# Kernel optimization log

Hardware: AMD Instinct MI355X
Metric: run time of the kernel (lower is better)

Reference implementation:

```python
import jax, jax.numpy as jnp
import numpy as np

B, NQ, L, E, K = 64, 1024, 128, 8192, 2
LN_EPS = 1e-5


def setup_inputs() -> dict:
    key = jax.random.key(0)
    ks = jax.random.split(key, 16)
    s1 = 1.0 / np.sqrt(2 * L + 1)
    s2 = 1.0 / np.sqrt(L)
    s3 = 1.0 / np.sqrt(2 * L)
    return {
        "z0": jax.random.normal(ks[0], (B, L), jnp.float32),
        "edge_index": jax.random.randint(ks[1], (2, E), 0, NQ, jnp.int64),
        "edge_attr": jax.random.normal(ks[2], (E,), jnp.float32),
        "n_qubits": NQ,
        # edge MLP params, stacked over K message-passing rounds
        "e_w1": jax.random.normal(ks[3], (K, L, 2 * L + 1), jnp.float32) * s1,
        "e_b1": jnp.zeros((K, L), jnp.float32),
        "e_w2": jax.random.normal(ks[4], (K, L, L), jnp.float32) * s2,
        "e_b2": jnp.zeros((K, L), jnp.float32),
        # node MLP params
        "n_w1": jax.random.normal(ks[5], (K, L, 2 * L), jnp.float32) * s3,
        "n_b1": jnp.zeros((K, L), jnp.float32),
        "ln_g": jnp.ones((K, L), jnp.float32),
        "ln_b": jnp.zeros((K, L), jnp.float32),
        "n_w2": jax.random.normal(ks[6], (K, L, L), jnp.float32) * s2,
        "n_b2": jnp.zeros((K, L), jnp.float32),
    }


def reference(z0, edge_index, edge_attr, n_qubits,
              e_w1, e_b1, e_w2, e_b2,
              n_w1, n_b1, ln_g, ln_b, n_w2, n_b2):
    b, l = z0.shape
    src, tgt = edge_index[0], edge_index[1]
    e_ = src.shape[0]
    # broadcast latent z0 to every node: h [B, N, L]
    h = jnp.broadcast_to(z0[:, None, :], (b, n_qubits, l))
    e = jnp.broadcast_to(edge_attr[None, :, None], (b, e_, 1))  # [B, E, 1]
    k_rounds = e_w1.shape[0]
    for k in range(k_rounds):
        hi = h[:, src, :]  # gather source node feats [B, E, L]
        hj = h[:, tgt, :]  # gather target node feats [B, E, L]
        inp_e = jnp.concatenate([hi, hj, e], axis=-1)  # [B, E, 2L+1]
        m = jax.nn.relu(inp_e @ e_w1[k].T + e_b1[k]) @ e_w2[k].T + e_b2[k]
        # scatter_add messages back to source nodes
        m_agg = jnp.zeros_like(h).at[:, src, :].add(m)
        inp_n = jnp.concatenate([h, m_agg], axis=-1)  # [B, N, 2L]
        x = jax.nn.relu(inp_n @ n_w1[k].T + n_b1[k])
        mu = x.mean(axis=-1, keepdims=True)
        var = ((x - mu) ** 2).mean(axis=-1, keepdims=True)
        x = (x - mu) * jax.lax.rsqrt(var + LN_EPS) * ln_g[k] + ln_b[k]
        # Dropout(p=0.1) is identity in eval mode
        h = x @ n_w2[k].T + n_b2[k] + h  # residual
    return h.mean(axis=1)  # [B, L]
```

## Files before the change

kernel.cpp:

```cpp
#include <hip/hip_runtime.h>

#define B_   64
#define NQ_  1024
#define L_   128
#define E_   8192
#define M_   (B_*NQ_)
#define LDP  136
#define TILE 2176

typedef unsigned short u16;
typedef unsigned int   u32;
typedef __attribute__((ext_vector_type(8))) short short8;
typedef __attribute__((ext_vector_type(4))) float floatx4;

#define WVB() __builtin_amdgcn_wave_barrier()

__device__ __forceinline__ u16 f2bf(float f) {
    union { float f; u32 u; } v; v.f = f;
    return (u16)((v.u + 0x7fffu + ((v.u >> 16) & 1u)) >> 16);
}
__device__ __forceinline__ float bf2f(u16 u) {
    union { u32 u; float f; } v; v.u = ((u32)u) << 16;
    return v.f;
}
__device__ __forceinline__ floatx4 mfma16(short8 a, short8 b, floatx4 c) {
    return __builtin_amdgcn_mfma_f32_16x16x32_bf16(a, b, c, 0, 0, 0);
}
__device__ __forceinline__ short8 gfrag(const u16* base, int r0, int kb, int lane) {
    return *(const short8*)(base + (size_t)(r0 + (lane & 15)) * 128 + kb * 32 + (lane >> 4) * 8);
}
__device__ __forceinline__ short8 sfrag(const u16* t, int r0, int kb, int lane) {
    return *(const short8*)(t + (r0 + (lane & 15)) * LDP + kb * 32 + (lane >> 4) * 8);
}
__device__ __forceinline__ short8 wfrag(const u16* wf, int nt, int kb, int lane) {
    return *(const short8*)(wf + (((kb << 3) + nt) * 64 + lane) * 8);
}
__device__ __forceinline__ void frag_flush(const u16* t, u16* wf, int nt, int lane) {
#pragma unroll
    for (int kb = 0; kb < 4; ++kb)
        *(short8*)(wf + (((kb << 3) + nt) * 64 + lane) * 8) = sfrag(t, 0, kb, lane);
}
__device__ __forceinline__ short8 frag_cvt(const float* base, int r0, int ld, int kb, int lane) {
    const float* p = base + (size_t)(r0 + (lane & 15)) * ld + kb * 32 + (lane >> 4) * 8;
    short8 s;
#pragma unroll
    for (int j = 0; j < 8; ++j) s[j] = (short)f2bf(p[j]);
    return s;
}
__device__ __forceinline__ void tile_store(u16* t, const floatx4* acc, int lane) {
    int col = lane & 15, qd = lane >> 4;
#pragma unroll
    for (int nt = 0; nt < 8; ++nt)
#pragma unroll
        for (int r = 0; r < 4; ++r)
            t[(qd * 4 + r) * LDP + nt * 16 + col] = f2bf(acc[nt][r]);
}
__device__ __forceinline__ void tile_flush(const u16* t, u16* g, int lane) {
#pragma unroll
    for (int it = 0; it < 4; ++it) {
        int chunk = it * 64 + lane, row = chunk >> 4, c8 = chunk & 15;
        *(uint4*)(g + (size_t)row * 128 + c8 * 8) = *(const uint4*)(t + row * LDP + c8 * 8);
    }
}

struct P {
    const int* ei; const float* attr; const float* z0;
    const float* e_w1; const float* e_b1; const float* e_w2; const float* e_b2;
    const float* n_w1; const float* n_b1; const float* ln_g; const float* ln_b;
    const float* n_w2; const float* n_b2;
    int* ofs; int* tgt_s; float* a_s; float* degf;
    u16* wf;
    u16* w_n20;
    float* wl; float* vb2;
    float* rx; float* rci; float* rcj; float* rh; float* mx0;
    u16* c0t; u16* S; u16* t1g; u16* ci1; u16* cj1;
    float* out;
};

__global__ __launch_bounds__(256) void k_setup(P p) {
    __shared__ __align__(16) char smem[52224];
    int tid = threadIdx.x, blk = blockIdx.x;
    int lane = tid & 63, w = tid >> 6, col = lane & 15, qd = lane >> 4;

    if (blk == 0) {
        int* cnt  = (int*)smem;
        int* wsum = cnt + 1024;
        int* flag = wsum + 8;
#pragma unroll
        for (int i = 0; i < 4; ++i) cnt[tid + i * 256] = 0;
        if (tid == 0) *flag = 1;
        __syncthreads();
        if (tid < 100 && p.ei[2 * tid + 1] != 0) atomicAnd(flag, 0);
        __syncthreads();
        int i64 = *flag;
        for (int e = tid; e < E_; e += 256) {
            int s = i64 ? p.ei[2 * e] : p.ei[e];
            atomicAdd(&cnt[s], 1);
        }
        __syncthreads();
        int q0 = tid * 4;
        int c0 = cnt[q0], c1 = cnt[q0 + 1], c2 = cnt[q0 + 2], c3 = cnt[q0 + 3];
        int tsum = c0 + c1 + c2 + c3, incl = tsum;
#pragma unroll
        for (int o = 1; o < 64; o <<= 1) {
            int t = __shfl_up(incl, o, 64);
            if (lane >= o) incl += t;
        }
        if (lane == 63) wsum[w] = incl;
        __syncthreads();
        int wo = 0;
        for (int i = 0; i < w; ++i) wo += wsum[i];
        int base = wo + incl - tsum;
        p.ofs[q0] = base; p.ofs[q0 + 1] = base + c0;
        p.ofs[q0 + 2] = base + c0 + c1; p.ofs[q0 + 3] = base + c0 + c1 + c2;
        p.degf[q0] = (float)c0; p.degf[q0 + 1] = (float)c1;
        p.degf[q0 + 2] = (float)c2; p.degf[q0 + 3] = (float)c3;
        if (tid == 0) p.ofs[NQ_] = E_;
        __syncthreads();
        cnt[q0] = base; cnt[q0 + 1] = base + c0;
        cnt[q0 + 2] = base + c0 + c1; cnt[q0 + 3] = base + c0 + c1 + c2;
        __syncthreads();
        for (int e = tid; e < E_; e += 256) {
            int s = i64 ? p.ei[2 * e]        : p.ei[e];
            int t = i64 ? p.ei[2 * (E_ + e)] : p.ei[E_ + e];
            int pos = atomicAdd(&cnt[s], 1);
            p.tgt_s[pos] = t;
            p.a_s[pos]   = p.attr[e];
        }
    } else if (blk == 1) {
        for (int idx = tid; idx < 16384; idx += 256) p.w_n20[idx] = f2bf(p.n_w2[idx]);
    } else if (blk == 2) {
        const float* src = p.n_w2 + 16384;
        u16* dst = p.wf + 5 * 16384;
        for (int pr = w; pr < 32; pr += 4) {
            int kb = pr >> 3, nt = pr & 7;
            const float* s = src + (nt * 16 + (lane & 15)) * 128 + kb * 32 + (lane >> 4) * 8;
            short8 v;
#pragma unroll
            for (int j = 0; j < 8; ++j) v[j] = (short)f2bf(s[j]);
            *(short8*)(dst + (pr * 64 + lane) * 8) = v;
        }
    } else if (blk <= 7) {
        const float* Pm; const float* Q; int ldp; u16* D;
        switch (blk) {
            case 3: Pm = p.n_w1 + 128;             ldp = 256; Q = p.e_w2;         D = p.wf;             break;
            case 4: Pm = p.n_w1 + 32768 + 128;     ldp = 256; Q = p.e_w2 + 16384; D = p.wf + 4 * 16384; break;
            case 5: Pm = p.e_w1 + 128 * 257;       ldp = 257; Q = p.n_w2;         D = p.wf + 1 * 16384; break;
            case 6: Pm = p.e_w1 + 128 * 257 + 128; ldp = 257; Q = p.n_w2;         D = p.wf + 2 * 16384; break;
            default:Pm = p.n_w1 + 32768;           ldp = 256; Q = p.n_w2;         D = p.wf + 3 * 16384; break;
        }
        u16* qt = (u16*)smem;
        u16* tl = (u16*)(smem + 34816);
        for (int idx = tid; idx < 16384; idx += 256) {
            int c = idx >> 7, kd = idx & 127;
            qt[kd * LDP + c] = f2bf(Q[idx]);
        }
        __syncthreads();
        for (int t = 0; t < 2; ++t) {
            int r0 = (w * 2 + t) * 16;
            floatx4 acc[8] = {};
#pragma unroll
            for (int kb = 0; kb < 4; ++kb) {
                short8 a = frag_cvt(Pm, r0, ldp, kb, lane);
#pragma unroll
                for (int nt = 0; nt < 8; ++nt)
                    acc[nt] = mfma16(a, sfrag(qt, nt * 16, kb, lane), acc[nt]);
            }
            u16* slot = tl + w * TILE;
            tile_store(slot, acc, lane); WVB();
            frag_flush(slot, D, w * 2 + t, lane); WVB();
        }
    } else if (blk == 8) {
        int r0 = w * 16;
        floatx4 acc[8] = {};
#pragma unroll
        for (int kb = 0; kb < 4; ++kb) {
            short8 a = frag_cvt(p.z0, r0, 128, kb, lane);
#pragma unroll
            for (int nt = 0; nt < 8; ++nt)
                acc[nt] = mfma16(a, frag_cvt(p.n_w1, nt * 16, 256, kb, lane), acc[nt]);
        }
#pragma unroll
        for (int nt = 0; nt < 8; ++nt) {
            int cg = nt * 16 + col; float bv = p.n_b1[cg];
#pragma unroll
            for (int r = 0; r < 4; ++r) p.rx[(r0 + qd * 4 + r) * 128 + cg] = acc[nt][r] + bv;
        }
    } else if (blk <= 11) {
        int r0 = w * 16;
        const float* Wp; int ld; const float* bias; float* dst;
        if (blk == 9)       { Wp = p.e_w1 + 128 * 257;       ld = 257; bias = p.e_b1 + 128; dst = p.rci; }
        else if (blk == 10) { Wp = p.e_w1 + 128 * 257 + 128; ld = 257; bias = nullptr;      dst = p.rcj; }
        else                { Wp = p.n_w1 + 32768;           ld = 256; bias = p.n_b1 + 128; dst = p.rh;  }
        floatx4 acc[8] = {};
#pragma unroll
        for (int kb = 0; kb < 4; ++kb) {
            short8 a;
            int rr = (r0 + (lane & 15)) * 128, kk = kb * 32 + (lane >> 4) * 8;
#pragma unroll
            for (int j = 0; j < 8; ++j) a[j] = (short)f2bf(p.z0[rr + kk + j] + p.n_b2[kk + j]);
#pragma unroll
            for (int nt = 0; nt < 8; ++nt)
                acc[nt] = mfma16(a, frag_cvt(Wp, nt * 16, ld, kb, lane), acc[nt]);
        }
#pragma unroll
        for (int nt = 0; nt < 8; ++nt) {
            int cg = nt * 16 + col;
            float bv = bias ? bias[cg] : 0.0f;
#pragma unroll
            for (int r = 0; r < 4; ++r) dst[(r0 + qd * 4 + r) * 128 + cg] = acc[nt][r] + bv;
        }
    } else if (blk == 12) {
        u16* tl = (u16*)(smem + 34816);
        int r0 = w * 16;
        floatx4 a1[8] = {};
#pragma unroll
        for (int kb = 0; kb < 4; ++kb) {
            short8 a = frag_cvt(p.z0, r0, 128, kb, lane);
#pragma unroll
            for (int nt = 0; nt < 8; ++nt) {
                a1[nt] = mfma16(a, frag_cvt(p.e_w1,       nt * 16, 257, kb, lane), a1[nt]);
                a1[nt] = mfma16(a, frag_cvt(p.e_w1 + 128, nt * 16, 257, kb, lane), a1[nt]);
            }
        }
#pragma unroll
        for (int nt = 0; nt < 8; ++nt) {
            float bv = p.e_b1[nt * 16 + col];
#pragma unroll
            for (int r = 0; r < 4; ++r) a1[nt][r] += bv;
        }
        u16* slot = tl + w * TILE;
        tile_store(slot, a1, lane); WVB();
        tile_flush(slot, p.c0t + (size_t)r0 * 128, lane);
    } else if (blk == 13) {
        int k = tid >> 7, c = tid & 127;
        float s = 0.0f;
        for (int n = 0; n < 128; ++n)
            s += p.n_w1[k * 32768 + c * 256 + 128 + n] * p.e_b2[k * 128 + n];
        p.vb2[tid] = s;
        p.wl[tid]  = p.e_w1[k * 128 * 257 + c * 257 + 256];
        for (int i = tid; i < 8192; i += 256) p.mx0[i] = 0.0f;
    }
}

__global__ __launch_bounds__(256) void k_edge(P p) {
    int tid = threadIdx.x, lane = tid & 63, w = tid >> 6;
    const float* wl = p.wl + 128;
    float2 wl2 = ((const float2*)wl)[lane];
    int gw = blockIdx.x * 4 + w;
    int q = gw & (NQ_ - 1), bg = gw >> 10;
    int bl[8];
#pragma unroll
    for (int i = 0; i < 4; ++i) { bl[i] = bg * 4 + i; bl[i + 4] = bg * 4 + i + 32; }
    int st = p.ofs[q], en = p.ofs[q + 1];
    float ax[8] = {}, ay[8] = {};
    const u32* cjp[8];
    float cx[8], cy[8];
#pragma unroll
    for (int i = 0; i < 8; ++i) {
        cjp[i] = (const u32*)p.cj1 + (size_t)bl[i] * NQ_ * 64;
        u32 cv = ((const u32*)p.ci1)[((size_t)bl[i] * NQ_ + q) * 64 + lane];
        cx[i] = bf2f((u16)(cv & 0xffff)); cy[i] = bf2f((u16)(cv >> 16));
    }
    for (int idx = st; idx < en; ++idx) {
        int t = p.tgt_s[idx];
        float a = p.a_s[idx];
        size_t ro = (size_t)t * 64 + lane;
        float wx = a * wl2.x, wy = a * wl2.y;
#pragma unroll
        for (int i = 0; i < 8; ++i) {
            u32 jv = cjp[i][ro];
            ax[i] += fmaxf(cx[i] + bf2f((u16)(jv & 0xffff)) + wx, 0.f);
            ay[i] += fmaxf(cy[i] + bf2f((u16)(jv >> 16))    + wy, 0.f);
        }
    }
    u32* Sp = (u32*)p.S;
#pragma unroll
    for (int i = 0; i < 8; ++i)
        Sp[((size_t)bl[i] * NQ_ + q) * 64 + lane] =
            (u32)f2bf(ax[i]) | ((u32)f2bf(ay[i]) << 16);
}

__global__ __launch_bounds__(256, 2) void k_node0(P p) {
    __shared__ __align__(16) char smem[52224];
    u16* xt = (u16*)smem;
    u16* ob = (u16*)(smem + 34816);
    int tid = threadIdx.x, lane = tid & 63, w = tid >> 6;
    int col = lane & 15, qd = lane >> 4;
    int blk = blockIdx.x;
    int rowbase = blk * 128 + w * 32;
    int b = blk >> 3;

    short8 af[2][4];
    {
        float wlf[4][8], c0f[4][8];
#pragma unroll
        for (int kb = 0; kb < 4; ++kb) {
            const float* wp = p.wl + kb * 32 + qd * 8;
            const u16*  cp = p.c0t + b * 128 + kb * 32 + qd * 8;
#pragma unroll
            for (int j = 0; j < 8; ++j) { wlf[kb][j] = wp[j]; c0f[kb][j] = bf2f(cp[j]); }
        }
#pragma unroll
        for (int t = 0; t < 2; ++t) {
            int q = (rowbase + t * 16 + col) & (NQ_ - 1);
            int st = p.ofs[q], en = p.ofs[q + 1];
            float Sv[4][8] = {};
            for (int idx = st; idx < en; ++idx) {
                float a = p.a_s[idx];
#pragma unroll
                for (int kb = 0; kb < 4; ++kb)
#pragma unroll
                    for (int j = 0; j < 8; ++j)
                        Sv[kb][j] += fmaxf(fmaf(a, wlf[kb][j], c0f[kb][j]), 0.f);
            }
#pragma unroll
            for (int kb = 0; kb < 4; ++kb) {
                short8 v;
#pragma unroll
                for (int j = 0; j < 8; ++j) v[j] = (short)f2bf(Sv[kb][j]);
                af[t][kb] = v;
            }
        }
    }

    floatx4 xa[2][8] = {};
#pragma unroll
    for (int kb = 0; kb < 4; ++kb) {
        short8 Bv[8];
#pragma unroll
        for (int nt = 0; nt < 8; ++nt) Bv[nt] = wfrag(p.wf, nt, kb, lane);
#pragma unroll
        for (int t = 0; t < 2; ++t)
#pragma unroll
            for (int nt = 0; nt < 8; ++nt) xa[t][nt] = mfma16(af[t][kb], Bv[nt], xa[t][nt]);
    }
    float s8[8] = {};
#pragma unroll
    for (int t = 0; t < 2; ++t) {
#pragma unroll
        for (int nt = 0; nt < 8; ++nt) {
            int cg = nt * 16 + col;
            float base = p.rx[b * 128 + cg], vb = p.vb2[cg];
#pragma unroll
            for (int r = 0; r < 4; ++r) {
                int row = rowbase + t * 16 + qd * 4 + r;
                xa[t][nt][r] = fmaxf(xa[t][nt][r] + base + p.degf[row & (NQ_ - 1)] * vb, 0.f);
            }
        }
#pragma unroll
        for (int r = 0; r < 4; ++r) {
            float s = 0.f, s2 = 0.f;
#pragma unroll
            for (int nt = 0; nt < 8; ++nt) { float v = xa[t][nt][r]; s += v; s2 += v * v; }
#pragma unroll
            for (int o = 1; o < 16; o <<= 1) { s += __shfl_xor(s, o, 64); s2 += __shfl_xor(s2, o, 64); }
            float mu = s * (1.f / 128.f), var = s2 * (1.f / 128.f) - mu * mu;
            float rs = rsqrtf(var + 1e-5f);
#pragma unroll
            for (int nt = 0; nt < 8; ++nt) {
                int cg = nt * 16 + col;
                float xv = (xa[t][nt][r] - mu) * rs * p.ln_g[cg] + p.ln_b[cg];
                xa[t][nt][r] = xv;
                s8[nt] += xv;
            }
        }
        tile_store(xt + (w * 2 + t) * TILE, xa[t], lane);
    }
#pragma unroll
    for (int nt = 0; nt < 8; ++nt) {
        s8[nt] += __shfl_xor(s8[nt], 16, 64);
        s8[nt] += __shfl_xor(s8[nt], 32, 64);
    }
    if (lane < 16) {
#pragma unroll
        for (int nt = 0; nt < 8; ++nt)
            atomicAdd(p.mx0 + b * 128 + nt * 16 + lane, s8[nt]);
    }
    WVB();
#pragma unroll
    for (int ph = 0; ph < 3; ++ph) {
        const u16* wfp = p.wf + ((ph == 0) ? 1 : (ph == 1) ? 2 : 3) * 16384;
        const float* rt = (ph == 0) ? p.rci : (ph == 1) ? p.rcj : p.rh;
        floatx4 ca[2][8] = {};
#pragma unroll
        for (int kb = 0; kb < 4; ++kb) {
            short8 Bv[8];
#pragma unroll
            for (int nt = 0; nt < 8; ++nt) Bv[nt] = wfrag(wfp, nt, kb, lane);
#pragma unroll
            for (int t = 0; t < 2; ++t) {
                short8 a = sfrag(xt + (w * 2 + t) * TILE, 0, kb, lane);
#pragma unroll
                for (int nt = 0; nt < 8; ++nt) ca[t][nt] = mfma16(a, Bv[nt], ca[t][nt]);
            }
        }
#pragma unroll
        for (int t = 0; t < 2; ++t)
#pragma unroll
            for (int nt = 0; nt < 8; ++nt) {
                float rc = rt[b * 128 + nt * 16 + col];
#pragma unroll
                for (int r = 0; r < 4; ++r) ca[t][nt][r] += rc;
            }
        u16* dst = (ph == 0) ? p.ci1 : (ph == 1) ? p.cj1 : p.t1g;
#pragma unroll
        for (int t = 0; t < 2; ++t) {
            tile_store(ob + w * TILE, ca[t], lane);
            WVB();
            tile_flush(ob + w * TILE, dst + (size_t)(rowbase + t * 16) * 128, lane);
            WVB();
        }
    }
}

__global__ __launch_bounds__(256, 2) void k_node1(P p) {
    __shared__ __align__(16) char smem[52224];
    u16* ob = (u16*)(smem + 34816);
    int tid = threadIdx.x, lane = tid & 63, w = tid >> 6;
    int col = lane & 15, qd = lane >> 4;
    int blk = blockIdx.x;
    int rowbase = blk * 128 + w * 32;
    int b = blk >> 3;

    const u16* wc1 = p.wf + 4 * 16384;
    floatx4 xa[2][8] = {};
#pragma unroll
    for (int kb = 0; kb < 4; ++kb) {
        short8 Bv[8];
#pragma unroll
        for (int nt = 0; nt < 8; ++nt) Bv[nt] = wfrag(wc1, nt, kb, lane);
#pragma unroll
        for (int t = 0; t < 2; ++t) {
            short8 a = gfrag(p.S, rowbase + t * 16, kb, lane);
#pragma unroll
            for (int nt = 0; nt < 8; ++nt) xa[t][nt] = mfma16(a, Bv[nt], xa[t][nt]);
        }
    }
    const float* vb21 = p.vb2 + 128;
#pragma unroll
    for (int t = 0; t < 2; ++t) {
#pragma unroll
        for (int nt = 0; nt < 8; ++nt) {
            int cg = nt * 16 + col;
            float vb = vb21[cg];
#pragma unroll
            for (int r = 0; r < 4; ++r) {
                int row = rowbase + t * 16 + qd * 4 + r;
                float tv = bf2f(p.t1g[(size_t)row * 128 + cg]);
                xa[t][nt][r] = fmaxf(xa[t][nt][r] + tv + p.degf[row & (NQ_ - 1)] * vb, 0.f);
            }
        }
#pragma unroll
        for (int r = 0; r < 4; ++r) {
            float s = 0.f, s2 = 0.f;
#pragma unroll
            for (int nt = 0; nt < 8; ++nt) { float v = xa[t][nt][r]; s += v; s2 += v * v; }
#pragma unroll
            for (int o = 1; o < 16; o <<= 1) { s += __shfl_xor(s, o, 64); s2 += __shfl_xor(s2, o, 64); }
            float mu = s * (1.f / 128.f), var = s2 * (1.f / 128.f) - mu * mu;
            float rs = rsqrtf(var + 1e-5f);
#pragma unroll
            for (int nt = 0; nt < 8; ++nt) {
                int cg = nt * 16 + col;
                xa[t][nt][r] = (xa[t][nt][r] - mu) * rs * p.ln_g[128 + cg] + p.ln_b[128 + cg];
            }
        }
    }
    const u16* n21 = p.wf + 5 * 16384;
    float s8[8] = {};
#pragma unroll
    for (int t = 0; t < 2; ++t) {
        WVB();
        tile_store(ob + w * TILE, xa[t], lane);
        WVB();
        floatx4 ma[8] = {};
#pragma unroll
        for (int kb = 0; kb < 4; ++kb) {
            short8 Bv[8];
#pragma unroll
            for (int nt = 0; nt < 8; ++nt) Bv[nt] = wfrag(n21, nt, kb, lane);
            short8 a = sfrag(ob + w * TILE, 0, kb, lane);
#pragma unroll
            for (int nt = 0; nt < 8; ++nt) ma[nt] = mfma16(a, Bv[nt], ma[nt]);
        }
#pragma unroll
        for (int nt = 0; nt < 8; ++nt)
#pragma unroll
            for (int r = 0; r < 4; ++r) s8[nt] += ma[nt][r];
    }
#pragma unroll
    for (int nt = 0; nt < 8; ++nt) {
        s8[nt] += __shfl_xor(s8[nt], 16, 64);
        s8[nt] += __shfl_xor(s8[nt], 32, 64);
    }
    if (lane < 16) {
#pragma unroll
        for (int nt = 0; nt < 8; ++nt)
            atomicAdd(p.out + b * 128 + nt * 16 + lane, s8[nt] * (1.f / 1024.f));
    }
    if ((blk & 7) == 0 && tid < 128) {
        int c = tid;
        const float* mx = p.mx0 + b * 128;
        float s = 0.f;
#pragma unroll 4
        for (int k = 0; k < 128; ++k) s += mx[k] * bf2f(p.w_n20[c * 128 + k]);
        float acc = p.z0[b * 128 + c] + p.n_b2[c] + p.n_b2[128 + c] + s * (1.f / 1024.f);
        atomicAdd(p.out + b * 128 + c, acc);
    }
}

extern "C" void kernel_launch(void* const* d_in, const int* in_sizes, int n_in,
                              void* d_out, int out_size, void* d_ws, size_t ws_size,
                              hipStream_t stream) {
    P p;
    p.z0   = (const float*)d_in[0];
    p.ei   = (const int*)d_in[1];
    p.attr = (const float*)d_in[2];
    p.e_w1 = (const float*)d_in[4];
    p.e_b1 = (const float*)d_in[5];
    p.e_w2 = (const float*)d_in[6];
    p.e_b2 = (const float*)d_in[7];
    p.n_w1 = (const float*)d_in[8];
    p.n_b1 = (const float*)d_in[9];
    p.ln_g = (const float*)d_in[10];
    p.ln_b = (const float*)d_in[11];
    p.n_w2 = (const float*)d_in[12];
    p.n_b2 = (const float*)d_in[13];
    p.out  = (float*)d_out;

    const size_t H = (size_t)M_ * L_;
    float* f  = (float*)d_ws;
    p.degf = f;
    p.a_s  = f + 1024;
    p.wl   = p.a_s + 8192;
    p.vb2  = p.wl + 256;
    p.rx   = p.vb2 + 256;
    p.rci  = p.rx + 8192;
    p.rcj  = p.rci + 8192;
    p.rh   = p.rcj + 8192;
    p.mx0  = p.rh + 8192;
    p.ofs  = (int*)(p.mx0 + 8192);
    p.tgt_s = p.ofs + 1056;
    p.wf    = (u16*)(p.tgt_s + 8192);
    p.w_n20 = p.wf + 6 * 16384;
    p.c0t   = p.w_n20 + 16384;
    p.S     = p.c0t + 8192;
    p.t1g   = p.S + H;
    p.ci1   = p.t1g + H;
    p.cj1   = p.ci1 + H;

    hipMemsetAsync(p.out, 0, 8192 * sizeof(float), stream);

    k_setup<<<14, 256, 0, stream>>>(p);
    k_node0<<<512, 256, 0, stream>>>(p);
    k_edge<<<2048, 256, 0, stream>>>(p);
    k_node1<<<512, 256, 0, stream>>>(p);
}
```

Baseline: 191.7 us.

## Split setup work across more blocks and restructure node0 edge aggregation via LDS

The setup kernel grows from 14 to 20 blocks. The weight-product GEMMs are each split across two blocks, and the Q operand is now read directly from global memory rather than staged through shared memory. The bias-vector dot product is vectorized with float4, and the final mx·W reduction reads packed bf16 vectors. In node0, each lane now accumulates two feature columns per row across edges and writes the result to an LDS tile. The MFMA A operand is then read from that tile, replacing the per-lane 32-element register accumulation. The aim is to shorten the serial setup critical path and cut register pressure in node0, at the cost of more serial loop iterations per lane and extra LDS traffic.

```diff
diff --git a/kernel.cpp b/kernel.cpp
--- a/kernel.cpp
+++ b/kernel.cpp
@@ -78,21 +78,21 @@
 };
 
 __global__ __launch_bounds__(256) void k_setup(P p) {
-    __shared__ __align__(16) char smem[52224];
+    __shared__ __align__(16) char smem[17408];
     int tid = threadIdx.x, blk = blockIdx.x;
     int lane = tid & 63, w = tid >> 6, col = lane & 15, qd = lane >> 4;
 
     if (blk == 0) {
-        int* cnt  = (int*)smem;
-        int* wsum = cnt + 1024;
-        int* flag = wsum + 8;
+        __shared__ int cnt[1024];
+        __shared__ int wsum[4];
+        __shared__ int flag;
 #pragma unroll
         for (int i = 0; i < 4; ++i) cnt[tid + i * 256] = 0;
-        if (tid == 0) *flag = 1;
+        if (tid == 0) flag = 1;
         __syncthreads();
-        if (tid < 100 && p.ei[2 * tid + 1] != 0) atomicAnd(flag, 0);
+        if (tid < 100 && p.ei[2 * tid + 1] != 0) atomicAnd(&flag, 0);
         __syncthreads();
-        int i64 = *flag;
+        int i64 = flag;
         for (int e = tid; e < E_; e += 256) {
             int s = i64 ? p.ei[2 * e] : p.ei[e];
             atomicAdd(&cnt[s], 1);
@@ -127,50 +127,50 @@
             p.tgt_s[pos] = t;
             p.a_s[pos]   = p.attr[e];
         }
-    } else if (blk == 1) {
-        for (int idx = tid; idx < 16384; idx += 256) p.w_n20[idx] = f2bf(p.n_w2[idx]);
-    } else if (blk == 2) {
+    } else if (blk <= 2) {
+        int base = (blk - 1) * 8192;
+        for (int idx = tid; idx < 8192; idx += 256)
+            p.w_n20[base + idx] = f2bf(p.n_w2[base + idx]);
+    } else if (blk == 3) {
         const float* src = p.n_w2 + 16384;
         u16* dst = p.wf + 5 * 16384;
         for (int pr = w; pr < 32; pr += 4) {
             int kb = pr >> 3, nt = pr & 7;
-            const float* s = src + (nt * 16 + (lane & 15)) * 128 + kb * 32 + (lane >> 4) * 8;
+            const float* s = src + (nt * 16 + col) * 128 + kb * 32 + qd * 8;
             short8 v;
 #pragma unroll
             for (int j = 0; j < 8; ++j) v[j] = (short)f2bf(s[j]);
             *(short8*)(dst + (pr * 64 + lane) * 8) = v;
         }
-    } else if (blk <= 7) {
+    } else if (blk <= 13) {
+        int g = (blk - 4) >> 1, part = (blk - 4) & 1;
         const float* Pm; const float* Q; int ldp; u16* D;
-        switch (blk) {
-            case 3: Pm = p.n_w1 + 128;             ldp = 256; Q = p.e_w2;         D = p.wf;             break;
-            case 4: Pm = p.n_w1 + 32768 + 128;     ldp = 256; Q = p.e_w2 + 16384; D = p.wf + 4 * 16384; break;
-            case 5: Pm = p.e_w1 + 128 * 257;       ldp = 257; Q = p.n_w2;         D = p.wf + 1 * 16384; break;
-            case 6: Pm = p.e_w1 + 128 * 257 + 128; ldp = 257; Q = p.n_w2;         D = p.wf + 2 * 16384; break;
-            default:Pm = p.n_w1 + 32768;           ldp = 256; Q = p.n_w2;         D = p.wf + 3 * 16384; break;
-        }
-        u16* qt = (u16*)smem;
-        u16* tl = (u16*)(smem + 34816);
-        for (int idx = tid; idx < 16384; idx += 256) {
-            int c = idx >> 7, kd = idx & 127;
-            qt[kd * LDP + c] = f2bf(Q[idx]);
-        }
-        __syncthreads();
-        for (int t = 0; t < 2; ++t) {
-            int r0 = (w * 2 + t) * 16;
-            floatx4 acc[8] = {};
-#pragma unroll
-            for (int kb = 0; kb < 4; ++kb) {
-                short8 a = frag_cvt(Pm, r0, ldp, kb, lane);
-#pragma unroll
-                for (int nt = 0; nt < 8; ++nt)
-                    acc[nt] = mfma16(a, sfrag(qt, nt * 16, kb, lane), acc[nt]);
-            }
-            u16* slot = tl + w * TILE;
-            tile_store(slot, acc, lane); WVB();
-            frag_flush(slot, D, w * 2 + t, lane); WVB();
-        }
-    } else if (blk == 8) {
+        switch (g) {
+            case 0:  Pm = p.n_w1 + 128;             ldp = 256; Q = p.e_w2;         D = p.wf;             break;
+            case 1:  Pm = p.n_w1 + 32768 + 128;     ldp = 256; Q = p.e_w2 + 16384; D = p.wf + 4 * 16384; break;
+            case 2:  Pm = p.e_w1 + 128 * 257;       ldp = 257; Q = p.n_w2;         D = p.wf + 1 * 16384; break;
+            case 3:  Pm = p.e_w1 + 128 * 257 + 128; ldp = 257; Q = p.n_w2;         D = p.wf + 2 * 16384; break;
+            default: Pm = p.n_w1 + 32768;           ldp = 256; Q = p.n_w2;         D = p.wf + 3 * 16384; break;
+        }
+        int tile = part * 4 + w;
+        int r0 = tile * 16;
+        floatx4 acc[8] = {};
+#pragma unroll
+        for (int kb = 0; kb < 4; ++kb) {
+            short8 a = frag_cvt(Pm, r0, ldp, kb, lane);
+#pragma unroll
+            for (int nt = 0; nt < 8; ++nt) {
+                short8 bq;
+#pragma unroll
+                for (int j = 0; j < 8; ++j)
+                    bq[j] = (short)f2bf(Q[(kb * 32 + qd * 8 + j) * 128 + nt * 16 + col]);
+                acc[nt] = mfma16(a, bq, acc[nt]);
+            }
+        }
+        u16* slot = (u16*)smem + w * TILE;
+        tile_store(slot, acc, lane); WVB();
+        frag_flush(slot, D, tile, lane);
+    } else if (blk == 14) {
         int r0 = w * 16;
         floatx4 acc[8] = {};
 #pragma unroll
@@ -186,17 +186,17 @@
 #pragma unroll
             for (int r = 0; r < 4; ++r) p.rx[(r0 + qd * 4 + r) * 128 + cg] = acc[nt][r] + bv;
         }
-    } else if (blk <= 11) {
+    } else if (blk <= 17) {
         int r0 = w * 16;
         const float* Wp; int ld; const float* bias; float* dst;
-        if (blk == 9)       { Wp = p.e_w1 + 128 * 257;       ld = 257; bias = p.e_b1 + 128; dst = p.rci; }
-        else if (blk == 10) { Wp = p.e_w1 + 128 * 257 + 128; ld = 257; bias = nullptr;      dst = p.rcj; }
+        if (blk == 15)      { Wp = p.e_w1 + 128 * 257;       ld = 257; bias = p.e_b1 + 128; dst = p.rci; }
+        else if (blk == 16) { Wp = p.e_w1 + 128 * 257 + 128; ld = 257; bias = nullptr;      dst = p.rcj; }
         else                { Wp = p.n_w1 + 32768;           ld = 256; bias = p.n_b1 + 128; dst = p.rh;  }
         floatx4 acc[8] = {};
 #pragma unroll
         for (int kb = 0; kb < 4; ++kb) {
             short8 a;
-            int rr = (r0 + (lane & 15)) * 128, kk = kb * 32 + (lane >> 4) * 8;
+            int rr = (r0 + col) * 128, kk = kb * 32 + qd * 8;
 #pragma unroll
             for (int j = 0; j < 8; ++j) a[j] = (short)f2bf(p.z0[rr + kk + j] + p.n_b2[kk + j]);
 #pragma unroll
@@ -210,8 +210,7 @@
 #pragma unroll
             for (int r = 0; r < 4; ++r) dst[(r0 + qd * 4 + r) * 128 + cg] = acc[nt][r] + bv;
         }
-    } else if (blk == 12) {
-        u16* tl = (u16*)(smem + 34816);
+    } else if (blk == 18) {
         int r0 = w * 16;
         floatx4 a1[8] = {};
 #pragma unroll
@@ -229,15 +228,20 @@
 #pragma unroll
             for (int r = 0; r < 4; ++r) a1[nt][r] += bv;
         }
-        u16* slot = tl + w * TILE;
+        u16* slot = (u16*)smem + w * TILE;
         tile_store(slot, a1, lane); WVB();
         tile_flush(slot, p.c0t + (size_t)r0 * 128, lane);
-    } else if (blk == 13) {
+    } else {
         int k = tid >> 7, c = tid & 127;
-        float s = 0.0f;
-        for (int n = 0; n < 128; ++n)
-            s += p.n_w1[k * 32768 + c * 256 + 128 + n] * p.e_b2[k * 128 + n];
-        p.vb2[tid] = s;
+        const float4* wp = (const float4*)(p.n_w1 + k * 32768 + c * 256 + 128);
+        const float4* bp = (const float4*)(p.e_b2 + k * 128);
+        float s0 = 0.f, s1 = 0.f, s2 = 0.f, s3 = 0.f;
+#pragma unroll
+        for (int n4 = 0; n4 < 32; ++n4) {
+            float4 a = wp[n4], bv = bp[n4];
+            s0 += a.x * bv.x; s1 += a.y * bv.y; s2 += a.z * bv.z; s3 += a.w * bv.w;
+        }
+        p.vb2[tid] = (s0 + s1) + (s2 + s3);
         p.wl[tid]  = p.e_w1[k * 128 * 257 + c * 257 + 256];
         for (int i = tid; i < 8192; i += 256) p.mx0[i] = 0.0f;
     }
@@ -291,38 +295,27 @@
     int rowbase = blk * 128 + w * 32;
     int b = blk >> 3;
 
-    short8 af[2][4];
     {
-        float wlf[4][8], c0f[4][8];
-#pragma unroll
-        for (int kb = 0; kb < 4; ++kb) {
-            const float* wp = p.wl + kb * 32 + qd * 8;
-            const u16*  cp = p.c0t + b * 128 + kb * 32 + qd * 8;
-#pragma unroll
-            for (int j = 0; j < 8; ++j) { wlf[kb][j] = wp[j]; c0f[kb][j] = bf2f(cp[j]); }
-        }
+        u32 cv = ((const u32*)p.c0t)[b * 64 + lane];
+        float c0x = bf2f((u16)(cv & 0xffff)), c0y = bf2f((u16)(cv >> 16));
+        float2 wl2 = ((const float2*)p.wl)[lane];
 #pragma unroll
         for (int t = 0; t < 2; ++t) {
-            int q = (rowbase + t * 16 + col) & (NQ_ - 1);
-            int st = p.ofs[q], en = p.ofs[q + 1];
-            float Sv[4][8] = {};
-            for (int idx = st; idx < en; ++idx) {
-                float a = p.a_s[idx];
-#pragma unroll
-                for (int kb = 0; kb < 4; ++kb)
-#pragma unroll
-                    for (int j = 0; j < 8; ++j)
-                        Sv[kb][j] += fmaxf(fmaf(a, wlf[kb][j], c0f[kb][j]), 0.f);
-            }
-#pragma unroll
-            for (int kb = 0; kb < 4; ++kb) {
-                short8 v;
-#pragma unroll
-                for (int j = 0; j < 8; ++j) v[j] = (short)f2bf(Sv[kb][j]);
-                af[t][kb] = v;
-            }
-        }
-    }
+            u32* tslot = (u32*)(xt + (w * 2 + t) * TILE);
+            for (int r16 = 0; r16 < 16; ++r16) {
+                int q = (rowbase + t * 16 + r16) & (NQ_ - 1);
+                int st = p.ofs[q], en = p.ofs[q + 1];
+                float ax = 0.f, ay = 0.f;
+                for (int idx = st; idx < en; ++idx) {
+                    float a = p.a_s[idx];
+                    ax += fmaxf(fmaf(a, wl2.x, c0x), 0.f);
+                    ay += fmaxf(fmaf(a, wl2.y, c0y), 0.f);
+                }
+                tslot[r16 * 68 + lane] = (u32)f2bf(ax) | ((u32)f2bf(ay) << 16);
+            }
+        }
+    }
+    WVB();
 
     floatx4 xa[2][8] = {};
 #pragma unroll
@@ -331,10 +324,13 @@
 #pragma unroll
         for (int nt = 0; nt < 8; ++nt) Bv[nt] = wfrag(p.wf, nt, kb, lane);
 #pragma unroll
-        for (int t = 0; t < 2; ++t)
-#pragma unroll
-            for (int nt = 0; nt < 8; ++nt) xa[t][nt] = mfma16(af[t][kb], Bv[nt], xa[t][nt]);
-    }
+        for (int t = 0; t < 2; ++t) {
+            short8 a = sfrag(xt + (w * 2 + t) * TILE, 0, kb, lane);
+#pragma unroll
+            for (int nt = 0; nt < 8; ++nt) xa[t][nt] = mfma16(a, Bv[nt], xa[t][nt]);
+        }
+    }
+    WVB();
     float s8[8] = {};
 #pragma unroll
     for (int t = 0; t < 2; ++t) {
@@ -503,8 +499,13 @@
         int c = tid;
         const float* mx = p.mx0 + b * 128;
         float s = 0.f;
-#pragma unroll 4
-        for (int k = 0; k < 128; ++k) s += mx[k] * bf2f(p.w_n20[c * 128 + k]);
+#pragma unroll
+        for (int k8 = 0; k8 < 16; ++k8) {
+            short8 wv = *(const short8*)(p.w_n20 + c * 128 + k8 * 8);
+            const float* mxp = mx + k8 * 8;
+#pragma unroll
+            for (int j = 0; j < 8; ++j) s += mxp[j] * bf2f((u16)wv[j]);
+        }
         float acc = p.z0[b * 128 + c] + p.n_b2[c] + p.n_b2[128 + c] + s * (1.f / 1024.f);
         atomicAdd(p.out + b * 128 + c, acc);
     }
@@ -552,7 +553,7 @@
 
     hipMemsetAsync(p.out, 0, 8192 * sizeof(float), stream);
 
-    k_setup<<<14, 256, 0, stream>>>(p);
+    k_setup<<<20, 256, 0, stream>>>(p);
     k_node0<<<512, 256, 0, stream>>>(p);
     k_edge<<<2048, 256, 0, stream>>>(p);
     k_node1<<<512, 256, 0, stream>>>(p);
```

New measurement: 202.7 us. +5.7%, slower.
